# Kernel tuning notes

Measured on AMD Instinct MI355X. Metric: run time of the kernel, lower is better.

Reference implementation:

```python
import jax, jax.numpy as jnp
import numpy as np

V, D_EMB, H, N_LAYERS = 50257, 512, 1024, 2
B, T = 8, 512


def setup_inputs() -> dict:
    key = jax.random.key(0)
    ks = jax.random.split(key, 9)
    s = 0.02
    return {
        "x": jax.random.randint(ks[0], (B, T), 0, V),
        "y": jax.random.randint(ks[1], (B, T), 0, V),
        "E": jax.random.normal(ks[2], (V, D_EMB), jnp.float32) * s,
        "Wih0": jax.random.normal(ks[3], (D_EMB, H), jnp.float32) * s,
        "Whh0": jax.random.normal(ks[4], (H, H), jnp.float32) * s,
        "Wih1": jax.random.normal(ks[5], (H, H), jnp.float32) * s,
        "Whh1": jax.random.normal(ks[6], (H, H), jnp.float32) * s,
        "Wfc": jax.random.normal(ks[7], (H, V), jnp.float32) * s,
        "bfc": jnp.zeros((V,), jnp.float32),
    }


def _rnn_layer(x_tbd, Wih, Whh):
    # x_tbd: (T, B, Din) time-major; tanh Elman cell, no bias.
    h0 = jnp.zeros((x_tbd.shape[1], Whh.shape[0]), x_tbd.dtype)

    def step(h, x_t):
        h_new = jnp.tanh(x_t @ Wih + h @ Whh)
        return h_new, h_new

    h_last, ys = jax.lax.scan(step, h0, x_tbd)
    return ys, h_last  # ys: (T, B, H)


def reference(x, y, E, Wih0, Whh0, Wih1, Whh1, Wfc, bfc):
    xe = E[x]                              # (B, T, D_EMB) embedding gather
    xs = jnp.swapaxes(xe, 0, 1)            # (T, B, D_EMB)
    ys0, _ = _rnn_layer(xs, Wih0, Whh0)    # layer 0
    ys1, _ = _rnn_layer(ys0, Wih1, Whh1)   # layer 1
    feats = jnp.swapaxes(ys1, 0, 1)        # (B, T, H)
    logits = feats @ Wfc + bfc             # (B, T, V)
    # cross_entropy with ignore_index=-1 (mean over valid tokens)
    flat = logits.reshape(-1, logits.shape[-1])
    yf = y.reshape(-1)
    valid = yf != -1
    y_safe = jnp.where(valid, yf, 0)
    logp = jax.nn.log_softmax(flat, axis=-1)
    nll = -jnp.take_along_axis(logp, y_safe[:, None], axis=-1)[:, 0]
    loss = jnp.sum(jnp.where(valid, nll, 0.0)) / jnp.maximum(valid.sum(), 1)
    return logits, loss
```

## Files before the change

kernel.cpp:

```cpp
#include <hip/hip_runtime.h>


#define H_DIM 1024
#define B_SZ 8
#define T_SZ 512
#define V_SZ 50257
#define V_PAD 50304

typedef __attribute__((ext_vector_type(8))) short bf16x8;
typedef __attribute__((ext_vector_type(4))) float f32x4;

__device__ __forceinline__ unsigned short f2bf(float f) {
  unsigned int u = __float_as_uint(f);
  u += 0x7fffu + ((u >> 16) & 1u);
  return (unsigned short)(u >> 16);
}
__device__ __forceinline__ float bf2f(unsigned short h) {
  return __uint_as_float(((unsigned int)h) << 16);
}
__device__ __forceinline__ float ftanh(float x) {
  float e = __expf(2.f * x);
  return 1.f - 2.f / (e + 1.f);
}
__device__ __forceinline__ int aload32(const int* p) {
  return __hip_atomic_load(p, __ATOMIC_RELAXED, __HIP_MEMORY_SCOPE_AGENT);
}
__device__ __forceinline__ void astore32i(int* p, int v) {
  __hip_atomic_store(p, v, __ATOMIC_RELAXED, __HIP_MEMORY_SCOPE_AGENT);
}
__device__ __forceinline__ unsigned long long aload64(const void* p) {
  return __hip_atomic_load((const unsigned long long*)p, __ATOMIC_RELAXED,
                           __HIP_MEMORY_SCOPE_AGENT);
}
__device__ __forceinline__ void astore64(void* p, unsigned long long v) {
  __hip_atomic_store((unsigned long long*)p, v, __ATOMIC_RELAXED,
                     __HIP_MEMORY_SCOPE_AGENT);
}
__device__ __forceinline__ void gload_lds16(const void* g, void* l) {
  __builtin_amdgcn_global_load_lds(
      (const __attribute__((address_space(1))) void*)g,
      (__attribute__((address_space(3))) void*)l, 16, 0, 0);
}

__global__ __launch_bounds__(256) void k_transpose(
    const float* __restrict__ in, unsigned short* __restrict__ out,
    int K, int N, int Npad)
{
  __shared__ float tile[32][33];
  const int n0 = blockIdx.x * 32, k0 = blockIdx.y * 32;
  const int tx = threadIdx.x, ty = threadIdx.y;
#pragma unroll
  for (int jj = 0; jj < 4; ++jj) {
    int k = k0 + ty + jj * 8, n = n0 + tx;
    tile[ty + jj * 8][tx] = (n < N) ? in[(size_t)k * N + n] : 0.f;
  }
  __syncthreads();
#pragma unroll
  for (int jj = 0; jj < 4; ++jj) {
    int n = n0 + ty + jj * 8, k = k0 + tx;
    if (n < Npad) out[(size_t)n * K + k] = f2bf((n < N) ? tile[tx][ty + jj * 8] : 0.f);
  }
}

__global__ __launch_bounds__(128) void k_embed(
    const int* __restrict__ x, const float* __restrict__ E,
    unsigned short* __restrict__ xe)
{
  const int r = blockIdx.x;
  const int t = r >> 3, b = r & 7;
  const int tok = x[b * T_SZ + t];
  const float4 v = ((const float4*)(E + (size_t)tok * 512))[threadIdx.x];
  ushort4 o;
  o.x = f2bf(v.x); o.y = f2bf(v.y); o.z = f2bf(v.z); o.w = f2bf(v.w);
  *((ushort4*)(xe + (size_t)r * 512) + threadIdx.x) = o;
}

template <bool BF16_OUT, bool BIAS>
__global__ __launch_bounds__(256) void k_gemm(
    const unsigned short* __restrict__ A, const unsigned short* __restrict__ Bt,
    void* __restrict__ Cout, const float* __restrict__ bias,
    int Nvalid, int K, int lda, int ldb, int ldc)
{
  __shared__ unsigned short As[8192];
  __shared__ unsigned short Bs[8192];
  const int tid = threadIdx.x;
  const int n0 = blockIdx.x * 128;
  const int m0 = blockIdx.y * 128;
  const int lane = tid & 63;
  const int wv = tid >> 6;
  const int wm = wv >> 1, wn = wv & 1;
  const int ln = lane & 15, cc = lane >> 4;
  f32x4 acc[4][4] = {};
  const int rr = tid >> 3;
  const int cb = (tid & 7) << 4;

  for (int kb = 0; kb < K; kb += 64) {
    __syncthreads();
#pragma unroll
    for (int is = 0; is < 4; ++is) {
      int r = is * 32 + rr;
      int sb = cb ^ ((r & 7) << 4);
      gload_lds16((const char*)(A + (size_t)(m0 + r) * lda + kb) + sb,
                  &As[(is * 32 + 8 * wv) * 64]);
    }
#pragma unroll
    for (int is = 0; is < 4; ++is) {
      int r = is * 32 + rr;
      int sb = cb ^ ((r & 7) << 4);
      gload_lds16((const char*)(Bt + (size_t)(n0 + r) * ldb + kb) + sb,
                  &Bs[(is * 32 + 8 * wv) * 64]);
    }
    __syncthreads();
#pragma unroll
    for (int kk = 0; kk < 2; ++kk) {
      bf16x8 af[4], bfr[4];
      const int kslot = kk * 64 + cc * 16;
#pragma unroll
      for (int mi = 0; mi < 4; ++mi) {
        int ra = wm * 64 + mi * 16 + ln;
        af[mi] = *(const bf16x8*)((const char*)As + ra * 128 + (kslot ^ ((ra & 7) << 4)));
      }
#pragma unroll
      for (int ni = 0; ni < 4; ++ni) {
        int rb = wn * 64 + ni * 16 + ln;
        bfr[ni] = *(const bf16x8*)((const char*)Bs + rb * 128 + (kslot ^ ((rb & 7) << 4)));
      }
#pragma unroll
      for (int mi = 0; mi < 4; ++mi)
#pragma unroll
        for (int ni = 0; ni < 4; ++ni)
          acc[mi][ni] = __builtin_amdgcn_mfma_f32_16x16x32_bf16(af[mi], bfr[ni], acc[mi][ni], 0, 0, 0);
    }
  }
#pragma unroll
  for (int ni = 0; ni < 4; ++ni) {
    const int col = n0 + wn * 64 + ni * 16 + ln;
    const bool cok = col < Nvalid;
    float bv = 0.f;
    if (BIAS && cok) bv = bias[col];
#pragma unroll
    for (int mi = 0; mi < 4; ++mi) {
#pragma unroll
      for (int i = 0; i < 4; ++i) {
        if (cok) {
          const int rowg = m0 + wm * 64 + mi * 16 + cc * 4 + i;
          if (BF16_OUT)
            ((unsigned short*)Cout)[(size_t)rowg * ldc + col] = f2bf(acc[mi][ni][i]);
          else
            ((float*)Cout)[(size_t)rowg * ldc + col] = acc[mi][ni][i] + bv;
        }
      }
    }
  }
}

template <int NQ>
__device__ __forceinline__ void gatherN(const uint2* __restrict__ sl,
    unsigned want, char* __restrict__ lds, int lane, int rowoff)
{
  unsigned long long v[NQ];
  for (;;) {
    bool ok = true;
#pragma unroll
    for (int q = 0; q < NQ; ++q)
      v[q] = aload64(sl + q * 64 + lane);
#pragma unroll
    for (int q = 0; q < NQ; ++q)
      ok &= ((unsigned)v[q] == want);
    if (__all(ok)) break;
  }
#pragma unroll
  for (int q = 0; q < NQ; ++q) {
    const int j = q * 64 + lane;
    const int row = rowoff + (j >> 9), kp = j & 511;
    *(unsigned*)(lds + ((row * 2048 + kp * 4) ^ ((row & 7) << 4))) =
        (unsigned)(v[q] >> 32);
  }
}

__device__ __forceinline__ void load_bw(bf16x8* bw, const float* W, int cc, int col)
{
#pragma unroll
  for (int kc = 0; kc < 32; ++kc) {
    const float* wp = W + (size_t)(kc * 32 + cc * 8) * H_DIM + col;
    bf16x8 v;
#pragma unroll
    for (int q = 0; q < 8; ++q) v[q] = (short)f2bf(wp[(size_t)q * H_DIM]);
    bw[kc] = v;
  }
}

__device__ __forceinline__ f32x4 mfma_k1024(const char* hs, const bf16x8* bw,
                                            int cc, int r)
{
  f32x4 ac0 = {}, ac1 = {};
  const int swz = r << 4;
#pragma unroll
  for (int kc = 0; kc < 32; kc += 2) {
    bf16x8 a0 = *(const bf16x8*)(hs + r * 2048 + ((kc * 64 + cc * 16) ^ swz));
    bf16x8 a1 = *(const bf16x8*)(hs + r * 2048 + (((kc + 1) * 64 + cc * 16) ^ swz));
    ac0 = __builtin_amdgcn_mfma_f32_16x16x32_bf16(a0, bw[kc], ac0, 0, 0, 0);
    ac1 = __builtin_amdgcn_mfma_f32_16x16x32_bf16(a1, bw[kc + 1], ac1, 0, 0, 0);
  }
  return ac0 + ac1;
}

__device__ void rec0(const unsigned short* U0, const float* Whh0,
    uint2* h0ring, const int* prog, char* smem, int wg)
{
  const int tid = threadIdx.x, lane = tid & 63, wv = tid >> 6;
  const int ln = lane & 15, cc = lane >> 4, r = ln & 7;
  const int col = wg * 64 + wv * 16 + ln;
  char* stage = smem;
  bf16x8 bw[32];
  load_bw(bw, Whh0, cc, col);
#pragma unroll 1
  for (int t = 0; t < T_SZ; ++t) {
    unsigned short uva[4] = {0, 0, 0, 0};
    if (cc < 2) {
#pragma unroll
      for (int i = 0; i < 4; ++i)
        uva[i] = U0[(size_t)(t * B_SZ + cc * 4 + i) * H_DIM + col];
    }
    gatherN<16>(h0ring + ((t + 3) & 3) * 4096 + wv * 1024, (unsigned)t,
                stage, lane, wv * 2);
    __syncthreads();
    f32x4 ac = mfma_k1024(stage, bw, cc, r);
    __syncthreads();
    float hv[4] = {0.f, 0.f, 0.f, 0.f};
    if (cc < 2) {
#pragma unroll
      for (int i = 0; i < 4; ++i) hv[i] = ftanh(ac[i] + bf2f(uva[i]));
    }
    unsigned wpk[4];
#pragma unroll
    for (int i = 0; i < 4; ++i) {
      float pv = __shfl_xor(hv[i], 1);
      wpk[i] = (unsigned)f2bf(hv[i]) | ((unsigned)f2bf(pv) << 16);
    }
    if (t >= 4) {
      const int* pp = prog + (lane & 31);
      while (!__all(aload32(pp) >= t - 3)) __builtin_amdgcn_s_sleep(1);
    }
    if (cc < 2 && !(ln & 1)) {
      uint2* outs = h0ring + (t & 3) * 4096;
      const int kp = col >> 1;
#pragma unroll
      for (int i = 0; i < 4; ++i)
        astore64(outs + (cc * 4 + i) * 512 + kp,
                 ((unsigned long long)wpk[i] << 32) | (unsigned long long)(t + 1));
    }
  }
}

__device__ void rec1(const float* Wih1, const float* Whh1,
    unsigned short* feats, uint2* h0ring, uint2* h1ring, int* prog,
    char* smem, int wg)
{
  const int tid = threadIdx.x, lane = tid & 63, wv = tid >> 6;
  const int ln = lane & 15, cc = lane >> 4, r = ln & 7;
  const int isB = wv >> 1;
  const int half = wv & 1;
  const int col = wg * 32 + half * 16 + ln;
  char* h0s = smem;
  char* h1s = smem + 16384;
  float* part = (float*)(smem + 32768);
  bf16x8 bw[32];
  load_bw(bw, isB ? Whh1 : Wih1, cc, col);
#pragma unroll 1
  for (int t = 0; t < T_SZ; ++t) {
    const uint2* ring = isB ? (h1ring + ((t + 3) & 3) * 4096)
                            : (h0ring + (t & 3) * 4096);
    char* stg = isB ? h1s : h0s;
    gatherN<32>(ring + half * 2048, (unsigned)(isB ? t : t + 1),
                stg, lane, half * 4);
    __syncthreads();
    f32x4 ac = mfma_k1024(isB ? h1s : h0s, bw, cc, r);
    if (!isB) *(f32x4*)(part + half * 256 + lane * 4) = ac;
    __syncthreads();
    if (isB) {
      f32x4 pa = *(const f32x4*)(part + half * 256 + lane * 4);
      float hv[4] = {0.f, 0.f, 0.f, 0.f};
      if (cc < 2) {
#pragma unroll
        for (int i = 0; i < 4; ++i) hv[i] = ftanh(ac[i] + pa[i]);
      }
      unsigned wpk[4];
#pragma unroll
      for (int i = 0; i < 4; ++i) {
        float pv = __shfl_xor(hv[i], 1);
        wpk[i] = (unsigned)f2bf(hv[i]) | ((unsigned)f2bf(pv) << 16);
      }
      if (cc < 2 && !(ln & 1)) {
        uint2* outs = h1ring + (t & 3) * 4096;
        const int kp = col >> 1;
#pragma unroll
        for (int i = 0; i < 4; ++i) {
          astore64(outs + (cc * 4 + i) * 512 + kp,
                   ((unsigned long long)wpk[i] << 32) | (unsigned long long)(t + 1));
          *(unsigned*)(feats + (size_t)(cc * 4 + i) * 524288 +
                       (size_t)t * 1024 + col) = wpk[i];
        }
      }
    }
    if (wv == 2 && lane == 0) astore32i(prog + wg, t + 1);
  }
}

__global__ __launch_bounds__(256, 1) void k_rectag(
    const unsigned short* __restrict__ U0,
    const float* __restrict__ Whh0, const float* __restrict__ Wih1,
    const float* __restrict__ Whh1, unsigned short* __restrict__ FEATS,
    uint2* __restrict__ h0ring, uint2* __restrict__ h1ring,
    int* __restrict__ prog)
{
  __shared__ __align__(16) char smem[34816];
  const int bid = blockIdx.x;
  if (bid < 16)
    rec0(U0, Whh0, h0ring, prog, smem, bid);
  else
    rec1(Wih1, Whh1, FEATS, h0ring, h1ring, prog, smem, bid - 16);
}

__global__ __launch_bounds__(256) void k_gemm_lse(
    const unsigned short* __restrict__ A, const unsigned short* __restrict__ Bt,
    float* __restrict__ C, const float* __restrict__ bias,
    float2* __restrict__ PARTg)
{
  __shared__ __align__(16) char smem[33792];
  unsigned short* As = (unsigned short*)smem;
  unsigned short* Bs = (unsigned short*)(smem + 16384);
  float2* lpart = (float2*)(smem + 32768);
  const int nb = blockIdx.x;
  const int m0 = blockIdx.y * 128, n0 = nb * 128;
  const int tid = threadIdx.x;
  const int lane = tid & 63;
  const int wv = tid >> 6;
  const int wm = wv >> 1, wn = wv & 1;
  const int ln = lane & 15, cc = lane >> 4;
  f32x4 acc[4][4] = {};
  const int rr = tid >> 3;
  const int cb = (tid & 7) << 4;

  for (int kb = 0; kb < H_DIM; kb += 64) {
    __syncthreads();
#pragma unroll
    for (int is = 0; is < 4; ++is) {
      int r = is * 32 + rr;
      int sb = cb ^ ((r & 7) << 4);
      gload_lds16((const char*)(A + (size_t)(m0 + r) * H_DIM + kb) + sb,
                  &As[(is * 32 + 8 * wv) * 64]);
    }
#pragma unroll
    for (int is = 0; is < 4; ++is) {
      int r = is * 32 + rr;
      int sb = cb ^ ((r & 7) << 4);
      gload_lds16((const char*)(Bt + (size_t)(n0 + r) * H_DIM + kb) + sb,
                  &Bs[(is * 32 + 8 * wv) * 64]);
    }
    __syncthreads();
#pragma unroll
    for (int kk = 0; kk < 2; ++kk) {
      bf16x8 af[4], bfr[4];
      const int kslot = kk * 64 + cc * 16;
#pragma unroll
      for (int mi = 0; mi < 4; ++mi) {
        int ra = wm * 64 + mi * 16 + ln;
        af[mi] = *(const bf16x8*)((const char*)As + ra * 128 + (kslot ^ ((ra & 7) << 4)));
      }
#pragma unroll
      for (int ni = 0; ni < 4; ++ni) {
        int rb = wn * 64 + ni * 16 + ln;
        bfr[ni] = *(const bf16x8*)((const char*)Bs + rb * 128 + (kslot ^ ((rb & 7) << 4)));
      }
#pragma unroll
      for (int mi = 0; mi < 4; ++mi)
#pragma unroll
        for (int ni = 0; ni < 4; ++ni)
          acc[mi][ni] = __builtin_amdgcn_mfma_f32_16x16x32_bf16(af[mi], bfr[ni], acc[mi][ni], 0, 0, 0);
    }
  }
  float bvn[4]; int ckn[4];
#pragma unroll
  for (int ni = 0; ni < 4; ++ni) {
    int col = n0 + wn * 64 + ni * 16 + ln;
    ckn[ni] = col < V_SZ;
    bvn[ni] = ckn[ni] ? bias[col] : 0.f;
  }
  float fm[16], fs[16];
#pragma unroll
  for (int mi = 0; mi < 4; ++mi) {
#pragma unroll
    for (int i = 0; i < 4; ++i) {
      float v[4];
#pragma unroll
      for (int ni = 0; ni < 4; ++ni) {
        float tv = acc[mi][ni][i] + bvn[ni];
        v[ni] = ckn[ni] ? tv : -1e30f;
        if (ckn[ni]) {
          int col = n0 + wn * 64 + ni * 16 + ln;
          C[(size_t)(m0 + wm * 64 + mi * 16 + cc * 4 + i) * V_SZ + col] = tv;
        }
      }
      float mx = fmaxf(fmaxf(v[0], v[1]), fmaxf(v[2], v[3]));
#pragma unroll
      for (int m = 1; m < 16; m <<= 1) mx = fmaxf(mx, __shfl_xor(mx, m));
      float se = __expf(v[0] - mx) + __expf(v[1] - mx) +
                 __expf(v[2] - mx) + __expf(v[3] - mx);
#pragma unroll
      for (int m = 1; m < 16; m <<= 1) se += __shfl_xor(se, m);
      fm[mi * 4 + i] = mx; fs[mi * 4 + i] = se;
    }
  }
  if (wn == 0 && ln == 0) {
#pragma unroll
    for (int mi = 0; mi < 4; ++mi)
#pragma unroll
      for (int i = 0; i < 4; ++i) {
        int rl = wm * 64 + mi * 16 + cc * 4 + i;
        lpart[rl] = make_float2(fm[mi * 4 + i], fs[mi * 4 + i]);
      }
  }
  __syncthreads();
  if (wn == 1 && ln == 0) {
#pragma unroll
    for (int mi = 0; mi < 4; ++mi)
#pragma unroll
      for (int i = 0; i < 4; ++i) {
        int rl = wm * 64 + mi * 16 + cc * 4 + i;
        float2 o = lpart[rl];
        float mx = fm[mi * 4 + i], se = fs[mi * 4 + i];
        float nm = fmaxf(mx, o.x);
        float S = se * __expf(mx - nm) + o.y * __expf(o.x - nm);
        PARTg[(size_t)(m0 + rl) * 393 + nb] = make_float2(nm, S);
      }
  }
}

__global__ __launch_bounds__(64) void k_loss_combine(
    const float2* __restrict__ PARTg, const float* __restrict__ logits,
    const int* __restrict__ y, float* __restrict__ rowloss)
{
  const int row = blockIdx.x, l = threadIdx.x;
  float M = -1e30f, S = 0.f;
  for (int i = l; i < 393; i += 64) {
    float2 p = PARTg[(size_t)row * 393 + i];
    float nm = fmaxf(M, p.x);
    S = S * __expf(M - nm) + p.y * __expf(p.x - nm);
    M = nm;
  }
#pragma unroll
  for (int off = 32; off > 0; off >>= 1) {
    float mo = __shfl_xor(M, off), so = __shfl_xor(S, off);
    float nm = fmaxf(M, mo);
    S = S * __expf(M - nm) + so * __expf(mo - nm);
    M = nm;
  }
  if (l == 0) {
    int tgt = y[row];
    float r = 0.f;
    if (tgt >= 0) r = M + __logf(S) - logits[(size_t)row * V_SZ + tgt];
    rowloss[row] = r;
  }
}

__global__ __launch_bounds__(256) void k_loss_final(
    const float* __restrict__ rowloss, const int* __restrict__ y,
    float* __restrict__ out)
{
  const int tid = threadIdx.x;
  float s = 0.f, c = 0.f;
  for (int i = tid; i < B_SZ * T_SZ; i += 256) {
    if (y[i] != -1) { s += rowloss[i]; c += 1.f; }
  }
  for (int off = 32; off > 0; off >>= 1) { s += __shfl_xor(s, off); c += __shfl_xor(c, off); }
  __shared__ float as_[4], ac_[4];
  const int wvi = tid >> 6, lnn = tid & 63;
  if (lnn == 0) { as_[wvi] = s; ac_[wvi] = c; }
  __syncthreads();
  if (tid == 0) {
    float S = as_[0] + as_[1] + as_[2] + as_[3];
    float C = ac_[0] + ac_[1] + ac_[2] + ac_[3];
    out[0] = S / fmaxf(C, 1.f);
  }
}

extern "C" void kernel_launch(void* const* d_in, const int* in_sizes, int n_in,
                              void* d_out, int out_size, void* d_ws, size_t ws_size,
                              hipStream_t stream) {
  (void)in_sizes; (void)n_in; (void)ws_size;
  const int* x = (const int*)d_in[0];
  const int* y = (const int*)d_in[1];
  const float* E = (const float*)d_in[2];
  const float* Wih0 = (const float*)d_in[3];
  const float* Whh0 = (const float*)d_in[4];
  const float* Wih1 = (const float*)d_in[5];
  const float* Whh1 = (const float*)d_in[6];
  const float* Wfc = (const float*)d_in[7];
  const float* bfc = (const float*)d_in[8];
  char* ws = (char*)d_ws;
  unsigned short* WfcT  = (unsigned short*)(ws + 0ULL);
  unsigned short* Wih0T = (unsigned short*)(ws + 103022592ULL);
  unsigned short* XE    = (unsigned short*)(ws + 104071168ULL);
  unsigned short* U0    = (unsigned short*)(ws + 108265472ULL);
  unsigned short* FEATS = (unsigned short*)(ws + 116654080ULL);
  float2* PART          = (float2*)(ws + 125042688ULL);
  float* ROWLOSS        = (float*)(ws + 137920512ULL);
  uint2* H0R            = (uint2*)(ws + 137936896ULL);
  uint2* H1R            = (uint2*)(ws + 138067968ULL);
  int* PROG             = (int*)(ws + 138199040ULL);
  float* logits = (float*)d_out;
  float* lossp = logits + (size_t)(out_size - 1);

  hipMemsetAsync(ws + 137936896ULL, 0, 262400, stream);

  k_transpose<<<dim3(32, 16), dim3(32, 8), 0, stream>>>(Wih0, Wih0T, 512, 1024, 1024);
  k_transpose<<<dim3(1572, 32), dim3(32, 8), 0, stream>>>(Wfc, WfcT, 1024, V_SZ, V_PAD);
  k_embed<<<4096, 128, 0, stream>>>(x, E, XE);
  k_gemm<true, false><<<dim3(8, 32), 256, 0, stream>>>(XE, Wih0T, U0, nullptr,
                                                       1024, 512, 512, 512, 1024);
  k_rectag<<<48, 256, 0, stream>>>(U0, Whh0, Wih1, Whh1, FEATS, H0R, H1R, PROG);
  k_gemm_lse<<<dim3(393, 32), 256, 0, stream>>>(FEATS, WfcT, logits, bfc, PART);
  k_loss_combine<<<4096, 64, 0, stream>>>(PART, logits, y, ROWLOSS);
  k_loss_final<<<1, 256, 0, stream>>>(ROWLOSS, y, lossp);
}
```

Measured before the change: 2.701 ms.

## Fuse recurrence and output GEMM into persistent kernel with progress-gated tile queue

Merges the two-layer recurrence kernel and the vocab projection GEMM+LSE kernel into one persistent launch of 512 blocks. 48 blocks run the recurrence at raised wave priority and publish per-block progress every 8 timesteps. The remaining blocks pull 128x128 GEMM tiles from an atomic counter, ordered by time chunk, and spin until the needed feature rows are written. The aim is to overlap the large logits GEMM with the latency-bound serial recurrence. The risks are contention for CUs and memory bandwidth that slows the critical recurrence path, plus spin-wait overhead.

```diff
diff --git a/kernel.cpp b/kernel.cpp
--- a/kernel.cpp
+++ b/kernel.cpp
@@ -6,6 +6,7 @@
 #define T_SZ 512
 #define V_SZ 50257
 #define V_PAD 50304
+#define NTILES 12576
 
 typedef __attribute__((ext_vector_type(8))) short bf16x8;
 typedef __attribute__((ext_vector_type(4))) float f32x4;
@@ -24,6 +25,9 @@
 }
 __device__ __forceinline__ int aload32(const int* p) {
   return __hip_atomic_load(p, __ATOMIC_RELAXED, __HIP_MEMORY_SCOPE_AGENT);
+}
+__device__ __forceinline__ void astore32(unsigned int* p, unsigned int v) {
+  __hip_atomic_store(p, v, __ATOMIC_RELAXED, __HIP_MEMORY_SCOPE_AGENT);
 }
 __device__ __forceinline__ void astore32i(int* p, int v) {
   __hip_atomic_store(p, v, __ATOMIC_RELAXED, __HIP_MEMORY_SCOPE_AGENT);
@@ -208,6 +212,7 @@
 __device__ void rec0(const unsigned short* U0, const float* Whh0,
     uint2* h0ring, const int* prog, char* smem, int wg)
 {
+  __builtin_amdgcn_s_setprio(1);
   const int tid = threadIdx.x, lane = tid & 63, wv = tid >> 6;
   const int ln = lane & 15, cc = lane >> 4, r = ln & 7;
   const int col = wg * 64 + wv * 16 + ln;
@@ -255,8 +260,9 @@
 
 __device__ void rec1(const float* Wih1, const float* Whh1,
     unsigned short* feats, uint2* h0ring, uint2* h1ring, int* prog,
-    char* smem, int wg)
-{
+    int* gprog, char* smem, int wg)
+{
+  __builtin_amdgcn_s_setprio(1);
   const int tid = threadIdx.x, lane = tid & 63, wv = tid >> 6;
   const int ln = lane & 15, cc = lane >> 4, r = ln & 7;
   const int isB = wv >> 1;
@@ -298,41 +304,28 @@
         for (int i = 0; i < 4; ++i) {
           astore64(outs + (cc * 4 + i) * 512 + kp,
                    ((unsigned long long)wpk[i] << 32) | (unsigned long long)(t + 1));
-          *(unsigned*)(feats + (size_t)(cc * 4 + i) * 524288 +
-                       (size_t)t * 1024 + col) = wpk[i];
+          astore32((unsigned*)(feats + (size_t)(cc * 4 + i) * 524288 +
+                               (size_t)t * 1024 + col), wpk[i]);
         }
       }
+      if ((t & 7) == 7) {
+        asm volatile("s_waitcnt vmcnt(0)" ::: "memory");
+        if (lane == 0) astore32i(gprog + (wg * 2 + half) * 32, t + 1);
+      }
     }
     if (wv == 2 && lane == 0) astore32i(prog + wg, t + 1);
   }
 }
 
-__global__ __launch_bounds__(256, 1) void k_rectag(
-    const unsigned short* __restrict__ U0,
-    const float* __restrict__ Whh0, const float* __restrict__ Wih1,
-    const float* __restrict__ Whh1, unsigned short* __restrict__ FEATS,
-    uint2* __restrict__ h0ring, uint2* __restrict__ h1ring,
-    int* __restrict__ prog)
-{
-  __shared__ __align__(16) char smem[34816];
-  const int bid = blockIdx.x;
-  if (bid < 16)
-    rec0(U0, Whh0, h0ring, prog, smem, bid);
-  else
-    rec1(Wih1, Whh1, FEATS, h0ring, h1ring, prog, smem, bid - 16);
-}
-
-__global__ __launch_bounds__(256) void k_gemm_lse(
-    const unsigned short* __restrict__ A, const unsigned short* __restrict__ Bt,
-    float* __restrict__ C, const float* __restrict__ bias,
-    float2* __restrict__ PARTg)
-{
-  __shared__ __align__(16) char smem[33792];
+__device__ void gemm_tile(const unsigned short* __restrict__ A,
+    const unsigned short* __restrict__ Bt, float* __restrict__ C,
+    const float* __restrict__ bias, float2* __restrict__ PARTg,
+    char* smem, int m0, int nb)
+{
   unsigned short* As = (unsigned short*)smem;
   unsigned short* Bs = (unsigned short*)(smem + 16384);
   float2* lpart = (float2*)(smem + 32768);
-  const int nb = blockIdx.x;
-  const int m0 = blockIdx.y * 128, n0 = nb * 128;
+  const int n0 = nb * 128;
   const int tid = threadIdx.x;
   const int lane = tid & 63;
   const int wv = tid >> 6;
@@ -435,6 +428,51 @@
         PARTg[(size_t)(m0 + rl) * 393 + nb] = make_float2(nm, S);
       }
   }
+}
+
+__device__ void worker_body(const unsigned short* FEATS,
+    const unsigned short* WfcT, const float* bias, float* C, float2* PARTg,
+    const int* gprog, int* TILE, char* smem)
+{
+  const int tid = threadIdx.x;
+  int* sT = (int*)(smem + 33792);
+  int passed = 0;
+  for (;;) {
+    __syncthreads();
+    if (tid == 0)
+      *sT = __hip_atomic_fetch_add(TILE, 1, __ATOMIC_RELAXED, __HIP_MEMORY_SCOPE_AGENT);
+    __syncthreads();
+    int id = *sT;
+    if (id >= NTILES) break;
+    int p = id / 3144, rem = id % 3144, nb = rem / 8, b = rem % 8;
+    int thr = 128 * (p + 1);
+    if (thr > passed) {
+      const int lane = tid & 63;
+      const int* gp = gprog + lane * 32;
+      while (!__all(aload32(gp) >= thr)) __builtin_amdgcn_s_sleep(32);
+      passed = thr;
+    }
+    gemm_tile(FEATS, WfcT, C, bias, PARTg, smem, b * 512 + p * 128, nb);
+  }
+}
+
+__global__ __launch_bounds__(256, 1) void k_mega(
+    const unsigned short* __restrict__ U0, const float* __restrict__ Whh0,
+    const float* __restrict__ Wih1, const float* __restrict__ Whh1,
+    unsigned short* __restrict__ FEATS, const unsigned short* __restrict__ WfcT,
+    const float* __restrict__ bfc, float* __restrict__ logits,
+    float2* __restrict__ PART, uint2* __restrict__ h0ring,
+    uint2* __restrict__ h1ring, int* __restrict__ prog,
+    int* __restrict__ gprog, int* __restrict__ TILE)
+{
+  __shared__ __align__(16) char smem[34816];
+  const int bid = blockIdx.x;
+  if (bid < 16)
+    rec0(U0, Whh0, h0ring, prog, smem, bid);
+  else if (bid < 48)
+    rec1(Wih1, Whh1, FEATS, h0ring, h1ring, prog, gprog, smem, bid - 16);
+  else
+    worker_body(FEATS, WfcT, bfc, logits, PART, gprog, TILE, smem);
 }
 
 __global__ __launch_bounds__(64) void k_loss_combine(
@@ -509,18 +547,20 @@
   uint2* H0R            = (uint2*)(ws + 137936896ULL);
   uint2* H1R            = (uint2*)(ws + 138067968ULL);
   int* PROG             = (int*)(ws + 138199040ULL);
+  int* GPROG            = (int*)(ws + 138199296ULL);
+  int* TILE             = (int*)(ws + 138207488ULL);
   float* logits = (float*)d_out;
   float* lossp = logits + (size_t)(out_size - 1);
 
-  hipMemsetAsync(ws + 137936896ULL, 0, 262400, stream);
+  hipMemsetAsync(ws + 137936896ULL, 0, 270848, stream);
 
   k_transpose<<<dim3(32, 16), dim3(32, 8), 0, stream>>>(Wih0, Wih0T, 512, 1024, 1024);
   k_transpose<<<dim3(1572, 32), dim3(32, 8), 0, stream>>>(Wfc, WfcT, 1024, V_SZ, V_PAD);
   k_embed<<<4096, 128, 0, stream>>>(x, E, XE);
   k_gemm<true, false><<<dim3(8, 32), 256, 0, stream>>>(XE, Wih0T, U0, nullptr,
                                                        1024, 512, 512, 512, 1024);
-  k_rectag<<<48, 256, 0, stream>>>(U0, Whh0, Wih1, Whh1, FEATS, H0R, H1R, PROG);
-  k_gemm_lse<<<dim3(393, 32), 256, 0, stream>>>(FEATS, WfcT, logits, bfc, PART);
+  k_mega<<<512, 256, 0, stream>>>(U0, Whh0, Wih1, Whh1, FEATS, WfcT, bfc,
+                                  logits, PART, H0R, H1R, PROG, GPROG, TILE);
   k_loss_combine<<<4096, 64, 0, stream>>>(PART, logits, y, ROWLOSS);
   k_loss_final<<<1, 256, 0, stream>>>(ROWLOSS, y, lossp);
 }
```

New measurement: 2.336 ms. -13.5%, faster.
